# Optimization experiments

Hardware: AMD Instinct MI355X
Metric: run time of the kernel (lower is better)

Reference implementation:

```python
import jax, jax.numpy as jnp
import numpy as np

INTERVAL = 0.02

def setup_inputs() -> dict:
    key = jax.random.key(0)
    ks = jax.random.split(key, 10)
    B, N, D, F = 8, 256, 64, 64
    return {
        "rbf_0": jax.random.normal(ks[0], (B, N, N, D), jnp.float32),
        "rbf_d": jax.random.normal(ks[1], (B, N, N, D), jnp.float32),
        "Q0_w": jax.random.normal(ks[2], (F, D), jnp.float32) * 0.1,
        "Q0_b": jax.random.normal(ks[3], (F,), jnp.float32) * 0.1,
        "Q_w": jax.random.normal(ks[4], (F, D), jnp.float32) * 0.1,
        "Q_b": jax.random.normal(ks[5], (F,), jnp.float32) * 0.1,
        "R0_w": jax.random.normal(ks[6], (F, D), jnp.float32) * 0.1,
        "R0_b": jax.random.normal(ks[7], (F,), jnp.float32) * 0.1,
        "R_w": jax.random.normal(ks[8], (F, D), jnp.float32) * 0.1,
        "R_b": jax.random.normal(ks[9], (F,), jnp.float32) * 0.1,
    }

def _linear(x, w, b):
    # x: [..., D], w: [F, D], b: [F] -> [..., F]
    return jnp.einsum('...d,fd->...f', x, w) + b

def reference(rbf_0, rbf_d, Q0_w, Q0_b, Q_w, Q_b, R0_w, R0_b, R_w, R_b):
    q_0 = _linear(rbf_0, Q0_w, Q0_b)   # [B, N, N, F]
    q = _linear(rbf_d, Q_w, Q_b)       # [B, N, N, F]
    r_0 = _linear(rbf_0, R0_w, R0_b)   # [B, N, N, F]
    r = _linear(rbf_d, R_w, R_b)       # [B, N, N, F]
    # 3-index correlator: contract over i and f
    C = jnp.einsum('bnif,bijf->bnj', q_0 * q, r_0 * r) * INTERVAL
    return C
```

## Files before the change

kernel.cpp:

```cpp
#include <hip/hip_runtime.h>
#include <hip/hip_bf16.h>


typedef __bf16 bf16x8 __attribute__((ext_vector_type(8)));
typedef float  f32x4  __attribute__((ext_vector_type(4)));
typedef int    i32x4  __attribute__((ext_vector_type(4)));
typedef unsigned short u16;
typedef u16    u16x8  __attribute__((ext_vector_type(8)));

static __device__ __forceinline__ __bf16 f2bf(float x) {
  union { __hip_bfloat16 h; __bf16 b; } u;
  u.h = __float2bfloat16(x);
  return u.b;
}
static __device__ __forceinline__ u16 f2bfu(float x) {
  union { __hip_bfloat16 h; u16 s; } u;
  u.h = __float2bfloat16(x);
  return u.s;
}
static __device__ __forceinline__ float bfu2f(u16 s) {
  union { unsigned int u; float f; } v;
  v.u = ((unsigned int)s) << 16;
  return v.f;
}
static __device__ __forceinline__ void gload16_nt(const float* gsrc, float* ldst) {
  __builtin_amdgcn_global_load_lds(
      (const __attribute__((address_space(1))) void*)gsrc,
      (__attribute__((address_space(3))) void*)ldst, 16, 0, 2);
}
static __device__ __forceinline__ void gload16u(const u16* gsrc, u16* ldst) {
  __builtin_amdgcn_global_load_lds(
      (const __attribute__((address_space(1))) void*)gsrc,
      (__attribute__((address_space(3))) void*)ldst, 16, 0, 0);
}

__global__ __launch_bounds__(256, 3) void k_phase1(
    const float* __restrict__ rbf0, const float* __restrict__ rbfd,
    const float* __restrict__ Q0w, const float* __restrict__ Q0b,
    const float* __restrict__ Qw,  const float* __restrict__ Qb,
    const float* __restrict__ R0w, const float* __restrict__ R0b,
    const float* __restrict__ Rw,  const float* __restrict__ Rb,
    u16* __restrict__ Aout, u16* __restrict__ Bout)
{
  __shared__ __align__(16) float lds[3][2][2048];

  const int tid  = threadIdx.x;
  const int lane = tid & 63;
  const int wave = tid >> 6;
  const int fr   = lane & 15;
  const int kg   = lane >> 4;
  const int role = wave >> 1;
  const int s    = wave & 1;

  const float* W0 = role ? R0w : Q0w;
  const float* W1 = role ? Rw  : Qw;
  const float* B0 = role ? R0b : Q0b;
  const float* B1 = role ? Rb  : Qb;
  u16* __restrict__ Out = role ? Bout : Aout;

  bf16x8 wf0[2][4], wf1[2][4];
#pragma unroll
  for (int kt = 0; kt < 2; ++kt)
#pragma unroll
    for (int ft = 0; ft < 4; ++ft) {
      const float* p0 = W0 + (ft * 16 + fr) * 64 + kt * 32 + kg * 8;
      const float* p1 = W1 + (ft * 16 + fr) * 64 + kt * 32 + kg * 8;
      f32x4 a = *(const f32x4*)p0, b = *(const f32x4*)(p0 + 4);
      f32x4 c = *(const f32x4*)p1, d = *(const f32x4*)(p1 + 4);
      bf16x8 w0v, w1v;
#pragma unroll
      for (int j = 0; j < 4; ++j) {
        w0v[j] = f2bf(a[j]); w0v[j + 4] = f2bf(b[j]);
        w1v[j] = f2bf(c[j]); w1v[j + 4] = f2bf(d[j]);
      }
      wf0[kt][ft] = w0v; wf1[kt][ft] = w1v;
    }

  u16x8 pb0[2], pb1[2];
#pragma unroll
  for (int ft = 0; ft < 4; ++ft)
#pragma unroll
    for (int r = 0; r < 4; ++r) {
      int idx = ft * 4 + r;
      pb0[idx >> 3][idx & 7] = f2bfu(B0[ft * 16 + kg * 4 + r]);
      pb1[idx >> 3][idx & 7] = f2bfu(B1[ft * 16 + kg * 4 + r]);
    }

  const int g0 = tid, g1 = 256 + tid;
  const int c0 = ((g0 >> 4) << 4) | ((g0 & 15) ^ ((g0 >> 4) & 15));
  const int c1 = ((g1 >> 4) << 4) | ((g1 & 15) ^ ((g1 >> 4) & 15));
  const int f0 = c0 * 4, f1 = c1 * 4;
  const int d0 = wave * 256, d1 = (wave + 4) * 256;

  const int bt0 = blockIdx.x;

#define S1_ISSUE(IT, SET)                                              \
  {                                                                    \
    const float* b0_ = rbf0 + (size_t)(bt0 + (IT) * 2048) * 2048;      \
    const float* b1_ = rbfd + (size_t)(bt0 + (IT) * 2048) * 2048;      \
    gload16_nt(b0_ + f0, &lds[SET][0][d0]);                            \
    gload16_nt(b0_ + f1, &lds[SET][0][d1]);                            \
    gload16_nt(b1_ + f0, &lds[SET][1][d0]);                            \
    gload16_nt(b1_ + f1, &lds[SET][1][d1]);                            \
  }

#define S1_COMPUTE(IT, SET)                                            \
  {                                                                    \
    const int row = s * 16 + fr;                                       \
    f32x4 ra[4], rb[4];                                                \
    _Pragma("unroll")                                                  \
    for (int kt = 0; kt < 2; ++kt)                                     \
      _Pragma("unroll")                                                \
      for (int h = 0; h < 2; ++h) {                                    \
        int c = kt * 8 + kg * 2 + h;                                   \
        int chunk = (row << 4) | (c ^ fr);                             \
        ra[kt * 2 + h] = *(const f32x4*)&lds[SET][0][chunk * 4];       \
        rb[kt * 2 + h] = *(const f32x4*)&lds[SET][1][chunk * 4];       \
      }                                                                \
    bf16x8 x0f[2], xdf[2];                                             \
    _Pragma("unroll")                                                  \
    for (int kt = 0; kt < 2; ++kt)                                     \
      _Pragma("unroll")                                                \
      for (int j = 0; j < 4; ++j) {                                    \
        x0f[kt][j]     = f2bf(ra[kt * 2][j]);                          \
        x0f[kt][j + 4] = f2bf(ra[kt * 2 + 1][j]);                      \
        xdf[kt][j]     = f2bf(rb[kt * 2][j]);                          \
        xdf[kt][j + 4] = f2bf(rb[kt * 2 + 1][j]);                      \
      }                                                                \
    f32x4 acc0[4], acc1[4];                                            \
    _Pragma("unroll")                                                  \
    for (int ft = 0; ft < 4; ++ft)                                     \
      _Pragma("unroll")                                                \
      for (int r = 0; r < 4; ++r) {                                    \
        int idx = ft * 4 + r;                                          \
        acc0[ft][r] = bfu2f(pb0[idx >> 3][idx & 7]);                   \
        acc1[ft][r] = bfu2f(pb1[idx >> 3][idx & 7]);                   \
      }                                                                \
    _Pragma("unroll")                                                  \
    for (int kt = 0; kt < 2; ++kt)                                     \
      _Pragma("unroll")                                                \
      for (int ft = 0; ft < 4; ++ft) {                                 \
        acc0[ft] = __builtin_amdgcn_mfma_f32_16x16x32_bf16(            \
            wf0[kt][ft], x0f[kt], acc0[ft], 0, 0, 0);                  \
        acc1[ft] = __builtin_amdgcn_mfma_f32_16x16x32_bf16(            \
            wf1[kt][ft], xdf[kt], acc1[ft], 0, 0, 0);                  \
      }                                                                \
    u16x8 o0, o1;                                                      \
    _Pragma("unroll")                                                  \
    for (int ft = 0; ft < 4; ++ft)                                     \
      _Pragma("unroll")                                                \
      for (int r = 0; r < 4; ++r) {                                    \
        int idx = ft * 4 + r;                                          \
        float v = acc0[ft][r] * acc1[ft][r];                           \
        if (idx < 8) o0[idx & 7] = f2bfu(v); else o1[idx & 7] = f2bfu(v); \
      }                                                                \
    u16* dst = Out + ((size_t)((bt0 + (IT) * 2048) * 32 + s * 16 + fr)) * 64 + kg * 16; \
    *(u16x8*)dst       = o0;                                           \
    *(u16x8*)(dst + 8) = o1;                                           \
  }

#define S1_ITER(IT, NWAIT, DO_ISSUE)                                   \
  {                                                                    \
    if (DO_ISSUE) S1_ISSUE((IT) + 2, ((IT) + 2) % 3);                  \
    asm volatile("s_waitcnt vmcnt(" #NWAIT ")" ::: "memory");          \
    __builtin_amdgcn_s_barrier();                                      \
    __builtin_amdgcn_sched_barrier(0);                                 \
    S1_COMPUTE(IT, (IT) % 3);                                          \
    asm volatile("s_waitcnt lgkmcnt(0)" ::: "memory");                 \
    __builtin_amdgcn_s_barrier();                                      \
    __builtin_amdgcn_sched_barrier(0);                                 \
  }

  S1_ISSUE(0, 0);
  S1_ISSUE(1, 1);

  S1_ITER(0,  8, 1);
  S1_ITER(1, 10, 1);
  S1_ITER(2, 12, 1);
  S1_ITER(3, 12, 1);
  S1_ITER(4, 12, 1);
  S1_ITER(5, 12, 1);
  S1_ITER(6,  8, 0);
  S1_ITER(7,  4, 0);

#undef S1_ITER
#undef S1_COMPUTE
#undef S1_ISSUE
}

__global__ __launch_bounds__(1024, 4) void k_phase2(
    const u16* __restrict__ A, const u16* __restrict__ Bm,
    float* __restrict__ C)
{
  __shared__ __align__(16) u16 As[2][16384];
  __shared__ __align__(16) u16 Bs[2][16384];

  const int tid  = threadIdx.x;
  const int lane = tid & 63;
  const int wave = tid >> 6;
  const int fr   = lane & 15;
  const int kg   = lane >> 4;
  const int wr   = wave >> 2;
  const int wc   = wave & 3;

  const int bid = blockIdx.x;
  const int kc  = bid & 31;
  const int b   = bid >> 5;
  const int i0  = kc * 8;

  const u16* Ab = A  + (size_t)b * 4194304;
  const u16* Bb = Bm + (size_t)b * 4194304;

  const int gA0 = wave * 64 + lane, gA1 = 1024 + gA0;
  const int r0 = gA0 >> 3, ch0 = gA0 & 7, cs0 = ch0 ^ (r0 & 7);
  const int r1 = gA1 >> 3, ch1 = gA1 & 7, cs1 = ch1 ^ (r1 & 7);
  const int rowA0 = r0 * 16384 + cs0 * 8;
  const int rowA1 = r1 * 16384 + cs1 * 8;
  const int rowB0 = r0 * 64 + cs0 * 8;
  const int rowB1 = r1 * 64 + cs1 * 8;
  const int dst0 = (wave * 64) * 8;
  const int dst1 = (1024 + wave * 64) * 8;

  f32x4 acc[4][4];
#pragma unroll
  for (int mt = 0; mt < 4; ++mt)
#pragma unroll
    for (int nn = 0; nn < 4; ++nn) {
      acc[mt][nn][0] = 0.f; acc[mt][nn][1] = 0.f;
      acc[mt][nn][2] = 0.f; acc[mt][nn][3] = 0.f;
    }

#define S2_ISSUE(I, BUF)                                               \
  {                                                                    \
    gload16u(Ab + rowA0 + (I) * 64, &As[BUF][dst0]);                   \
    gload16u(Ab + rowA1 + (I) * 64, &As[BUF][dst1]);                   \
    gload16u(Bb + rowB0 + (size_t)(I) * 16384, &Bs[BUF][dst0]);        \
    gload16u(Bb + rowB1 + (size_t)(I) * 16384, &Bs[BUF][dst1]);        \
  }

#define S2_COMPUTE(BUF)                                                \
  {                                                                    \
    _Pragma("unroll")                                                  \
    for (int kt = 0; kt < 2; ++kt) {                                   \
      bf16x8 af[4], bfv[4];                                            \
      _Pragma("unroll")                                                \
      for (int mt = 0; mt < 4; ++mt) {                                 \
        int row = wr * 64 + mt * 16 + fr;                              \
        int c = kt * 4 + kg;                                           \
        af[mt] = *(const bf16x8*)&As[BUF][row * 64 + ((c ^ (row & 7)) * 8)]; \
      }                                                                \
      _Pragma("unroll")                                                \
      for (int nn = 0; nn < 4; ++nn) {                                 \
        int row = wc * 64 + nn * 16 + fr;                              \
        int c = kt * 4 + kg;                                           \
        bfv[nn] = *(const bf16x8*)&Bs[BUF][row * 64 + ((c ^ (row & 7)) * 8)]; \
      }                                                                \
      _Pragma("unroll")                                                \
      for (int mt = 0; mt < 4; ++mt)                                   \
        _Pragma("unroll")                                              \
        for (int nn = 0; nn < 4; ++nn)                                 \
          acc[mt][nn] = __builtin_amdgcn_mfma_f32_16x16x32_bf16(       \
              af[mt], bfv[nn], acc[mt][nn], 0, 0, 0);                  \
    }                                                                  \
  }

#define S2_ITER(IT, NWAIT, DO_ISSUE)                                   \
  {                                                                    \
    if (DO_ISSUE) S2_ISSUE(i0 + (IT) + 1, ((IT) + 1) & 1);             \
    asm volatile("s_waitcnt vmcnt(" #NWAIT ")" ::: "memory");          \
    __builtin_amdgcn_s_barrier();                                      \
    __builtin_amdgcn_sched_barrier(0);                                 \
    S2_COMPUTE((IT) & 1);                                              \
    asm volatile("s_waitcnt lgkmcnt(0)" ::: "memory");                 \
    __builtin_amdgcn_s_barrier();                                      \
    __builtin_amdgcn_sched_barrier(0);                                 \
  }

  S2_ISSUE(i0, 0);

  S2_ITER(0, 4, 1);
  S2_ITER(1, 4, 1);
  S2_ITER(2, 4, 1);
  S2_ITER(3, 4, 1);
  S2_ITER(4, 4, 1);
  S2_ITER(5, 4, 1);
  S2_ITER(6, 4, 1);
  S2_ITER(7, 0, 0);

#undef S2_ITER
#undef S2_COMPUTE
#undef S2_ISSUE

  float* Cb = C + ((size_t)b << 16);
#pragma unroll
  for (int mt = 0; mt < 4; ++mt)
#pragma unroll
    for (int nn = 0; nn < 4; ++nn)
#pragma unroll
      for (int r = 0; r < 4; ++r) {
        int n = wr * 64 + mt * 16 + kg * 4 + r;
        int j = wc * 64 + nn * 16 + fr;
        atomicAdd(&Cb[n * 256 + j], acc[mt][nn][r] * 0.02f);
      }
}

extern "C" void kernel_launch(void* const* d_in, const int* in_sizes, int n_in,
                              void* d_out, int out_size, void* d_ws, size_t ws_size,
                              hipStream_t stream)
{
  const float* rbf0 = (const float*)d_in[0];
  const float* rbfd = (const float*)d_in[1];
  const float* Q0w  = (const float*)d_in[2];
  const float* Q0b  = (const float*)d_in[3];
  const float* Qw   = (const float*)d_in[4];
  const float* Qb   = (const float*)d_in[5];
  const float* R0w  = (const float*)d_in[6];
  const float* R0b  = (const float*)d_in[7];
  const float* Rw   = (const float*)d_in[8];
  const float* Rb   = (const float*)d_in[9];
  float* out = (float*)d_out;

  u16* Abuf = (u16*)d_ws;
  u16* Bbuf = Abuf + (size_t)33554432;

  hipMemsetAsync(d_out, 0, (size_t)out_size * sizeof(float), stream);
  hipLaunchKernelGGL(k_phase1, dim3(2048), dim3(256), 0, stream,
                     rbf0, rbfd, Q0w, Q0b, Qw, Qb, R0w, R0b, Rw, Rb, Abuf, Bbuf);
  hipLaunchKernelGGL(k_phase2, dim3(256), dim3(1024), 0, stream, Abuf, Bbuf, out);
}
```

Measured before the change: 169.4 us.

## Write phase-1 A output transposed so phase-2 loads both operands contiguously

Phase 1 now stores the q0*q product (role 0) with the n1/n2 indices swapped, so A is laid out as [b][i][n][f] like B. Phase 2 then loads A tiles with the same contiguous 16KB-per-i stride as B, instead of gathering rows that sit 16384 elements apart. The cost moves into phase 1, whose role-0 stores become scattered across rows instead of sequential.

```diff
diff --git a/kernel.cpp b/kernel.cpp
--- a/kernel.cpp
+++ b/kernel.cpp
@@ -23,7 +23,7 @@
   v.u = ((unsigned int)s) << 16;
   return v.f;
 }
-static __device__ __forceinline__ void gload16_nt(const float* gsrc, float* ldst) {
+static __device__ __forceinline__ void gload16_a2(const float* gsrc, float* ldst) {
   __builtin_amdgcn_global_load_lds(
       (const __attribute__((address_space(1))) void*)gsrc,
       (__attribute__((address_space(3))) void*)ldst, 16, 0, 2);
@@ -98,10 +98,10 @@
   {                                                                    \
     const float* b0_ = rbf0 + (size_t)(bt0 + (IT) * 2048) * 2048;      \
     const float* b1_ = rbfd + (size_t)(bt0 + (IT) * 2048) * 2048;      \
-    gload16_nt(b0_ + f0, &lds[SET][0][d0]);                            \
-    gload16_nt(b0_ + f1, &lds[SET][0][d1]);                            \
-    gload16_nt(b1_ + f0, &lds[SET][1][d0]);                            \
-    gload16_nt(b1_ + f1, &lds[SET][1][d1]);                            \
+    gload16_a2(b0_ + f0, &lds[SET][0][d0]);                            \
+    gload16_a2(b0_ + f1, &lds[SET][0][d1]);                            \
+    gload16_a2(b1_ + f0, &lds[SET][1][d0]);                            \
+    gload16_a2(b1_ + f1, &lds[SET][1][d1]);                            \
   }
 
 #define S1_COMPUTE(IT, SET)                                            \
@@ -154,7 +154,18 @@
         float v = acc0[ft][r] * acc1[ft][r];                           \
         if (idx < 8) o0[idx & 7] = f2bfu(v); else o1[idx & 7] = f2bfu(v); \
       }                                                                \
-    u16* dst = Out + ((size_t)((bt0 + (IT) * 2048) * 32 + s * 16 + fr)) * 64 + kg * 16; \
+     \
+    size_t p0 = (size_t)(bt0 + (IT) * 2048) * 32 + s * 16;             \
+    size_t dstoff;                                                     \
+    if (role) {                                                        \
+      dstoff = (p0 + fr) << 6;             \
+    } else {                                                           \
+      size_t b_  = p0 >> 16;                                           \
+      size_t n1_ = (p0 >> 8) & 255;                                    \
+      size_t n2_ = (p0 & 255) + fr;                                    \
+      dstoff = ((b_ << 16) | (n2_ << 8) | n1_) << 6;   \
+    }                                                                  \
+    u16* dst = Out + dstoff + kg * 16;                                 \
     *(u16x8*)dst       = o0;                                           \
     *(u16x8*)(dst + 8) = o1;                                           \
   }
@@ -211,15 +222,13 @@
   const u16* Ab = A  + (size_t)b * 4194304;
   const u16* Bb = Bm + (size_t)b * 4194304;
 
-  const int gA0 = wave * 64 + lane, gA1 = 1024 + gA0;
-  const int r0 = gA0 >> 3, ch0 = gA0 & 7, cs0 = ch0 ^ (r0 & 7);
-  const int r1 = gA1 >> 3, ch1 = gA1 & 7, cs1 = ch1 ^ (r1 & 7);
-  const int rowA0 = r0 * 16384 + cs0 * 8;
-  const int rowA1 = r1 * 16384 + cs1 * 8;
-  const int rowB0 = r0 * 64 + cs0 * 8;
-  const int rowB1 = r1 * 64 + cs1 * 8;
-  const int dst0 = (wave * 64) * 8;
-  const int dst1 = (1024 + wave * 64) * 8;
+  const int g0 = wave * 64 + lane, g1 = 1024 + g0;
+  const int r0 = g0 >> 3, sw0 = (g0 & 7) ^ (r0 & 7);
+  const int r1 = g1 >> 3, sw1 = (g1 & 7) ^ (r1 & 7);
+  const int off0 = r0 * 64 + sw0 * 8;
+  const int off1 = r1 * 64 + sw1 * 8;
+  const int dst0 = wave * 512;
+  const int dst1 = 8192 + wave * 512;
 
   f32x4 acc[4][4];
 #pragma unroll
@@ -232,10 +241,11 @@
 
 #define S2_ISSUE(I, BUF)                                               \
   {                                                                    \
-    gload16u(Ab + rowA0 + (I) * 64, &As[BUF][dst0]);                   \
-    gload16u(Ab + rowA1 + (I) * 64, &As[BUF][dst1]);                   \
-    gload16u(Bb + rowB0 + (size_t)(I) * 16384, &Bs[BUF][dst0]);        \
-    gload16u(Bb + rowB1 + (size_t)(I) * 16384, &Bs[BUF][dst1]);        \
+    const size_t tb = (size_t)(I) * 16384;                             \
+    gload16u(Ab + tb + off0, &As[BUF][dst0]);                          \
+    gload16u(Ab + tb + off1, &As[BUF][dst1]);                          \
+    gload16u(Bb + tb + off0, &Bs[BUF][dst0]);                          \
+    gload16u(Bb + tb + off1, &Bs[BUF][dst1]);                          \
   }
 
 #define S2_COMPUTE(BUF)                                                \
@@ -264,13 +274,13 @@
     }                                                                  \
   }
 
-#define S2_ITER(IT, NWAIT, DO_ISSUE)                                   \
-  {                                                                    \
-    if (DO_ISSUE) S2_ISSUE(i0 + (IT) + 1, ((IT) + 1) & 1);             \
+#define S2_ITER(T, NWAIT, DO_ISSUE)                                    \
+  {                                                                    \
+    if (DO_ISSUE) S2_ISSUE(i0 + (T) + 1, ((T) + 1) & 1);               \
     asm volatile("s_waitcnt vmcnt(" #NWAIT ")" ::: "memory");          \
     __builtin_amdgcn_s_barrier();                                      \
     __builtin_amdgcn_sched_barrier(0);                                 \
-    S2_COMPUTE((IT) & 1);                                              \
+    S2_COMPUTE((T) & 1);                                               \
     asm volatile("s_waitcnt lgkmcnt(0)" ::: "memory");                 \
     __builtin_amdgcn_s_barrier();                                      \
     __builtin_amdgcn_sched_barrier(0);                                 \
```

New measurement: 168.7 us. No clear change (-0.4%).
